# Optimization experiments

Hardware: AMD Instinct MI355X
Metric: run time of the kernel (lower is better)

Reference implementation:

```python
import jax, jax.numpy as jnp
import numpy as np

D, LEN_IN, LEN_OUT = 2, 1, 10
H1, H2 = 32, 32
B, T = 4096, 512
F_IN = D * LEN_IN          # 2
F_OUT = D * LEN_OUT        # 20


def setup_inputs() -> dict:
    key = jax.random.key(0)
    ks = jax.random.split(key, 12)
    s = 1.0 / np.sqrt(H1)  # PyTorch default init scale for LSTMCell/Linear
    u = lambda k, shape: jax.random.uniform(k, shape, jnp.float32, -s, s)
    return {
        "x": jax.random.normal(ks[0], (B, T, F_IN), jnp.float32),
        # LSTMCell 1 (input 2 -> hidden 32); gate order i,f,g,o stacked on dim 0
        "W_ih1": u(ks[1], (4 * H1, F_IN)),
        "W_hh1": u(ks[2], (4 * H1, H1)),
        "b_ih1": u(ks[3], (4 * H1,)),
        "b_hh1": u(ks[4], (4 * H1,)),
        # LSTMCell 2 (32 -> 32)
        "W_ih2": u(ks[5], (4 * H2, H1)),
        "W_hh2": u(ks[6], (4 * H2, H2)),
        "b_ih2": u(ks[7], (4 * H2,)),
        "b_hh2": u(ks[8], (4 * H2,)),
        # Final linear 32 -> 20
        "W_out": u(ks[9], (F_OUT, H2)),
        "b_out": u(ks[10], (F_OUT,)),
    }


def _lstm_cell(x, h, c, W_ih, W_hh, b):
    # gates: [B, 4H]; PyTorch gate order i, f, g, o
    gates = x @ W_ih.T + h @ W_hh.T + b
    i, f, g, o = jnp.split(gates, 4, axis=-1)
    i, f, o = jax.nn.sigmoid(i), jax.nn.sigmoid(f), jax.nn.sigmoid(o)
    g = jnp.tanh(g)
    c_new = f * c + i * g
    h_new = o * jnp.tanh(c_new)
    return h_new, c_new


def reference(x, W_ih1, W_hh1, b_ih1, b_hh1, W_ih2, W_hh2, b_ih2, b_hh2, W_out, b_out):
    b1 = b_ih1 + b_hh1
    b2 = b_ih2 + b_hh2
    Bsz = x.shape[0]
    h1 = jnp.zeros((Bsz, H1), x.dtype)
    c1 = jnp.zeros((Bsz, H1), x.dtype)
    h2 = jnp.zeros((Bsz, H2), x.dtype)
    c2 = jnp.zeros((Bsz, H2), x.dtype)

    def step(carry, x_t):
        h1, c1, h2, c2 = carry
        h1, c1 = _lstm_cell(x_t, h1, c1, W_ih1, W_hh1, b1)
        h2, c2 = _lstm_cell(h1, h2, c2, W_ih2, W_hh2, b2)
        out_t = h2 @ W_out.T + b_out  # [B, 20]
        return (h1, c1, h2, c2), out_t

    xs = jnp.swapaxes(x, 0, 1)  # [T, B, F_IN]
    _, outs = jax.lax.scan(step, (h1, c1, h2, c2), xs)  # outs: [T, B, 20]
    outs = jnp.swapaxes(outs, 0, 1)  # [B, T, 20]
    return outs.reshape(Bsz, x.shape[1], D, LEN_OUT)
```

## Files before the change

### kernel.cpp

```cpp
#include <hip/hip_runtime.h>
#include <hip/hip_fp16.h>

#define TLEN 512
#define HDIM 32
#define FOUT 20
#define HST  36

typedef __attribute__((ext_vector_type(8))) short bf16x8;
typedef __attribute__((ext_vector_type(4))) float f32x4;
typedef __attribute__((ext_vector_type(4))) short s16x4;

__device__ __forceinline__ float sigm(float v) {
  float e = __builtin_amdgcn_exp2f(-1.4426950408889634f * v);
  return __builtin_amdgcn_rcpf(1.0f + e);
}
__device__ __forceinline__ float tanh_f(float v) {
  float e = __builtin_amdgcn_exp2f(2.8853900817779268f * v);
  return 1.0f - 2.0f * __builtin_amdgcn_rcpf(1.0f + e);
}
__device__ __forceinline__ void hilo(float v, short& h, short& l) {
  unsigned u = __builtin_bit_cast(unsigned, v);
  unsigned r = u + 0x7fffu + ((u >> 16) & 1u);
  h = (short)(r >> 16);
  float hf = __builtin_bit_cast(float, r & 0xffff0000u);
  float res = v - hf;
  unsigned u2 = __builtin_bit_cast(unsigned, res);
  unsigned r2 = u2 + 0x7fffu + ((u2 >> 16) & 1u);
  l = (short)(r2 >> 16);
}

__device__ __forceinline__ void barrier_lgkm() {
  asm volatile("s_waitcnt lgkmcnt(0)\n\ts_barrier" ::: "memory");
}

__device__ __forceinline__ bf16x8 read_h(const short* buf, int off) {
  s16x4 a = *(const s16x4*)(buf + off);
  s16x4 b = *(const s16x4*)(buf + off + 4);
  bf16x8 r;
  r[0]=a[0]; r[1]=a[1]; r[2]=a[2]; r[3]=a[3];
  r[4]=b[0]; r[5]=b[1]; r[6]=b[2]; r[7]=b[3];
  return r;
}

__device__ __forceinline__ float lstm_update(const f32x4& g, float& c) {
  float iv = sigm(g[0]), fv = sigm(g[1]), gv = tanh_f(g[2]), ov = sigm(g[3]);
  c = fv * c + iv * gv;
  return ov * tanh_f(c);
}

__global__ __launch_bounds__(1024, 1) void lstm_seq_kernel(
    const float* __restrict__ xg,
    const float* __restrict__ Wih1, const float* __restrict__ Whh1,
    const float* __restrict__ bih1, const float* __restrict__ bhh1,
    const float* __restrict__ Wih2, const float* __restrict__ Whh2,
    const float* __restrict__ bih2, const float* __restrict__ bhh2,
    const float* __restrict__ Wout, const float* __restrict__ bout,
    float* __restrict__ out)
{
  __shared__ __half xl[16 * 1028];
  __shared__ short h1hiB[2][16 * HST], h1loB[2][16 * HST];
  __shared__ short h2hiB[2][16 * HST], h2loB[2][16 * HST];

  const int tid  = threadIdx.x;
  const int w    = tid >> 6;
  const int lane = tid & 63;
  const int n    = lane & 15;
  const int q    = lane >> 4;
  const int q4   = q * 4;
  const int q8   = q * 8;
  const int b0   = blockIdx.x * 16;
  const bool isL1 = (w < 8);
  const int wr   = w & 7;
  const int p    = w & 1;
  const int pr   = w >> 1;

  for (int idx = tid; idx < 16 * 1024; idx += 1024) {
    int row = idx >> 10, col = idx & 1023;
    xl[row * 1028 + col] = __float2half(xg[((size_t)(b0 + row) << 10) + col]);
  }

  const int og = (n & 3) * HDIM + 4 * wr + (n >> 2);
  bf16x8 WAh, WAl, WBh, WBl;
  float bc[4], wx0[4], wx1[4], boc[4];
  bf16x8 WoH = {0,0,0,0,0,0,0,0}, WoL = {0,0,0,0,0,0,0,0};
  if (isL1) {
    #pragma unroll
    for (int j = 0; j < 8; j++) {
      short hh, ll;
      hilo(Whh1[og * HDIM + q8 + j], hh, ll); WAh[j] = hh; WAl[j] = ll;
    }
    #pragma unroll
    for (int r = 0; r < 4; r++) {
      int gr = r * HDIM + 4 * wr + q;
      bc[r]  = bih1[gr] + bhh1[gr];
      wx0[r] = Wih1[gr * 2 + 0];
      wx1[r] = Wih1[gr * 2 + 1];
      int orow = 16 * p + q4 + r;
      boc[r] = (orow < FOUT) ? bout[orow] : 0.0f;
    }
    int orow = 16 * p + n;
    if (orow < FOUT) {
      #pragma unroll
      for (int j = 0; j < 8; j++) {
        short hh, ll;
        hilo(Wout[orow * HDIM + q8 + j], hh, ll); WoH[j] = hh; WoL[j] = ll;
      }
    }
  } else {
    #pragma unroll
    for (int j = 0; j < 8; j++) {
      short hh, ll;
      hilo(Wih2[og * HDIM + q8 + j], hh, ll); WAh[j] = hh; WAl[j] = ll;
      hilo(Whh2[og * HDIM + q8 + j], hh, ll); WBh[j] = hh; WBl[j] = ll;
    }
    #pragma unroll
    for (int r = 0; r < 4; r++) {
      int gr = r * HDIM + 4 * wr + q;
      bc[r] = bih2[gr] + bhh2[gr];
    }
  }

  const int hoff = n * HST + 4 * wr + q;
  const int aoff = n * HST + q8;
  float c = 0.0f;

  bf16x8 h1h = {0,0,0,0,0,0,0,0}, h1l = {0,0,0,0,0,0,0,0};
  bf16x8 h2h = {0,0,0,0,0,0,0,0}, h2l = {0,0,0,0,0,0,0,0};

  __syncthreads();

  if (isL1) {
    __half2 hv = *(const __half2*)&xl[n * 1028];
    float xv0 = __half2float(hv.x), xv1 = __half2float(hv.y);
    f32x4 g1;
    #pragma unroll
    for (int r = 0; r < 4; r++) g1[r] = fmaf(xv1, wx1[r], fmaf(xv0, wx0[r], bc[r]));
    float h1n = lstm_update(g1, c);
    short hh, ll; hilo(h1n, hh, ll);
    h1hiB[0][hoff] = hh; h1loB[0][hoff] = ll;
  }
  barrier_lgkm();
  h1h = read_h(h1hiB[0], aoff);
  h1l = read_h(h1loB[0], aoff);

  for (int t = 1; t < TLEN; ++t) {
    const int par = t & 1;
    if (isL1) {
      __half2 hv = *(const __half2*)&xl[n * 1028 + 2 * t];
      float xv0 = __half2float(hv.x), xv1 = __half2float(hv.y);

      f32x4 g1;
      #pragma unroll
      for (int r = 0; r < 4; r++) g1[r] = fmaf(xv1, wx1[r], fmaf(xv0, wx0[r], bc[r]));
      g1 = __builtin_amdgcn_mfma_f32_16x16x32_bf16(WAh, h1h, g1, 0, 0, 0);
      g1 = __builtin_amdgcn_mfma_f32_16x16x32_bf16(WAl, h1h, g1, 0, 0, 0);
      g1 = __builtin_amdgcn_mfma_f32_16x16x32_bf16(WAh, h1l, g1, 0, 0, 0);

      float h1n = lstm_update(g1, c);
      short hh, ll; hilo(h1n, hh, ll);
      h1hiB[par][hoff] = hh; h1loB[par][hoff] = ll;

      const int s = t - 2;
      if (s >= 0 && pr == (s & 3)) {
        f32x4 ao;
        #pragma unroll
        for (int r = 0; r < 4; r++) ao[r] = boc[r];
        ao = __builtin_amdgcn_mfma_f32_16x16x32_bf16(WoH, h2h, ao, 0, 0, 0);
        ao = __builtin_amdgcn_mfma_f32_16x16x32_bf16(WoL, h2h, ao, 0, 0, 0);
        ao = __builtin_amdgcn_mfma_f32_16x16x32_bf16(WoH, h2l, ao, 0, 0, 0);
        if (p == 0 || q == 0) {
          float4 st = { ao[0], ao[1], ao[2], ao[3] };
          *(float4*)&out[((size_t)(b0 + n) * TLEN + s) * FOUT + 16 * p + q4] = st;
        }
      }
    } else {
      f32x4 ga, gb;
      #pragma unroll
      for (int r = 0; r < 4; r++) { ga[r] = bc[r]; gb[r] = 0.0f; }
      ga = __builtin_amdgcn_mfma_f32_16x16x32_bf16(WAh, h1h, ga, 0, 0, 0);
      gb = __builtin_amdgcn_mfma_f32_16x16x32_bf16(WBh, h2h, gb, 0, 0, 0);
      ga = __builtin_amdgcn_mfma_f32_16x16x32_bf16(WAl, h1h, ga, 0, 0, 0);
      gb = __builtin_amdgcn_mfma_f32_16x16x32_bf16(WBl, h2h, gb, 0, 0, 0);
      ga = __builtin_amdgcn_mfma_f32_16x16x32_bf16(WAh, h1l, ga, 0, 0, 0);
      gb = __builtin_amdgcn_mfma_f32_16x16x32_bf16(WBh, h2l, gb, 0, 0, 0);

      f32x4 g2;
      #pragma unroll
      for (int r = 0; r < 4; r++) g2[r] = ga[r] + gb[r];
      float h2n = lstm_update(g2, c);
      short hh, ll; hilo(h2n, hh, ll);
      h2hiB[par][hoff] = hh; h2loB[par][hoff] = ll;
    }

    barrier_lgkm();

    h1h = read_h(h1hiB[par], aoff);
    h1l = read_h(h1loB[par], aoff);
    if (!isL1 || pr == ((t - 1) & 3)) {
      h2h = read_h(h2hiB[par], aoff);
      h2l = read_h(h2loB[par], aoff);
    }
  }

  if (!isL1) {
    f32x4 ga, gb;
    #pragma unroll
    for (int r = 0; r < 4; r++) { ga[r] = bc[r]; gb[r] = 0.0f; }
    ga = __builtin_amdgcn_mfma_f32_16x16x32_bf16(WAh, h1h, ga, 0, 0, 0);
    gb = __builtin_amdgcn_mfma_f32_16x16x32_bf16(WBh, h2h, gb, 0, 0, 0);
    ga = __builtin_amdgcn_mfma_f32_16x16x32_bf16(WAl, h1h, ga, 0, 0, 0);
    gb = __builtin_amdgcn_mfma_f32_16x16x32_bf16(WBl, h2h, gb, 0, 0, 0);
    ga = __builtin_amdgcn_mfma_f32_16x16x32_bf16(WAh, h1l, ga, 0, 0, 0);
    gb = __builtin_amdgcn_mfma_f32_16x16x32_bf16(WBh, h2l, gb, 0, 0, 0);
    f32x4 g2;
    #pragma unroll
    for (int r = 0; r < 4; r++) g2[r] = ga[r] + gb[r];
    float h2n = lstm_update(g2, c);
    short hh, ll; hilo(h2n, hh, ll);
    h2hiB[0][hoff] = hh; h2loB[0][hoff] = ll;
  } else if (pr == 2) {
    const int s = TLEN - 2;
    f32x4 ao;
    #pragma unroll
    for (int r = 0; r < 4; r++) ao[r] = boc[r];
    ao = __builtin_amdgcn_mfma_f32_16x16x32_bf16(WoH, h2h, ao, 0, 0, 0);
    ao = __builtin_amdgcn_mfma_f32_16x16x32_bf16(WoL, h2h, ao, 0, 0, 0);
    ao = __builtin_amdgcn_mfma_f32_16x16x32_bf16(WoH, h2l, ao, 0, 0, 0);
    if (p == 0 || q == 0) {
      float4 st = { ao[0], ao[1], ao[2], ao[3] };
      *(float4*)&out[((size_t)(b0 + n) * TLEN + s) * FOUT + 16 * p + q4] = st;
    }
  }
  barrier_lgkm();

  if (isL1 && pr == 3) {
    h2h = read_h(h2hiB[0], aoff);
    h2l = read_h(h2loB[0], aoff);
    const int s = TLEN - 1;
    f32x4 ao;
    #pragma unroll
    for (int r = 0; r < 4; r++) ao[r] = boc[r];
    ao = __builtin_amdgcn_mfma_f32_16x16x32_bf16(WoH, h2h, ao, 0, 0, 0);
    ao = __builtin_amdgcn_mfma_f32_16x16x32_bf16(WoL, h2h, ao, 0, 0, 0);
    ao = __builtin_amdgcn_mfma_f32_16x16x32_bf16(WoH, h2l, ao, 0, 0, 0);
    if (p == 0 || q == 0) {
      float4 st = { ao[0], ao[1], ao[2], ao[3] };
      *(float4*)&out[((size_t)(b0 + n) * TLEN + s) * FOUT + 16 * p + q4] = st;
    }
  }
}

extern "C" void kernel_launch(void* const* d_in, const int* in_sizes, int n_in,
                              void* d_out, int out_size, void* d_ws, size_t ws_size,
                              hipStream_t stream) {
  const float* xg   = (const float*)d_in[0];
  const float* Wih1 = (const float*)d_in[1];
  const float* Whh1 = (const float*)d_in[2];
  const float* bih1 = (const float*)d_in[3];
  const float* bhh1 = (const float*)d_in[4];
  const float* Wih2 = (const float*)d_in[5];
  const float* Whh2 = (const float*)d_in[6];
  const float* bih2 = (const float*)d_in[7];
  const float* bhh2 = (const float*)d_in[8];
  const float* Wout = (const float*)d_in[9];
  const float* bout = (const float*)d_in[10];
  float* out = (float*)d_out;

  hipLaunchKernelGGL(lstm_seq_kernel, dim3(256), dim3(1024), 0, stream,
                     xg, Wih1, Whh1, bih1, bhh1, Wih2, Whh2, bih2, bhh2, Wout, bout, out);
}
```

Baseline: 494.3 us.

## Unroll LSTM time loop by four and move output projection after barrier

The timestep loop is unrolled by four through a STEP macro, so parity and rotating-row indices become compile-time constants, and the x inputs for four steps come from two vector LDS loads. The hidden-state row stride grows from 36 to 40 shorts so each read_h becomes a single aligned 8-element LDS load instead of two 4-element loads. The output-projection MFMAs and global stores now run after the barrier instead of before it, taking them off the critical path to the barrier. The risks are higher register pressure and code size from the unrolling, and possible LDS bank conflicts from the new stride.

Result: faster. 442.4 us (-10.5%).

```diff
diff --git a/kernel.cpp b/kernel.cpp
--- a/kernel.cpp
+++ b/kernel.cpp
@@ -4,7 +4,7 @@
 #define TLEN 512
 #define HDIM 32
 #define FOUT 20
-#define HST  36
+#define HST  40
 
 typedef __attribute__((ext_vector_type(8))) short bf16x8;
 typedef __attribute__((ext_vector_type(4))) float f32x4;
@@ -34,12 +34,7 @@
 }
 
 __device__ __forceinline__ bf16x8 read_h(const short* buf, int off) {
-  s16x4 a = *(const s16x4*)(buf + off);
-  s16x4 b = *(const s16x4*)(buf + off + 4);
-  bf16x8 r;
-  r[0]=a[0]; r[1]=a[1]; r[2]=a[2]; r[3]=a[3];
-  r[4]=b[0]; r[5]=b[1]; r[6]=b[2]; r[7]=b[3];
-  return r;
+  return *(const bf16x8*)(buf + off);
 }
 
 __device__ __forceinline__ float lstm_update(const f32x4& g, float& c) {
@@ -143,64 +138,82 @@
   h1h = read_h(h1hiB[0], aoff);
   h1l = read_h(h1loB[0], aoff);
 
-  for (int t = 1; t < TLEN; ++t) {
-    const int par = t & 1;
+#define STEP(T, PAR, DS3, HR3, XV0, XV1)                                          \
+  {                                                                               \
+    if (isL1) {                                                                   \
+      f32x4 g1;                                                                   \
+      _Pragma("unroll") for (int r = 0; r < 4; r++)                               \
+        g1[r] = fmaf((XV1), wx1[r], fmaf((XV0), wx0[r], bc[r]));                  \
+      g1 = __builtin_amdgcn_mfma_f32_16x16x32_bf16(WAh, h1h, g1, 0, 0, 0);        \
+      g1 = __builtin_amdgcn_mfma_f32_16x16x32_bf16(WAl, h1h, g1, 0, 0, 0);        \
+      g1 = __builtin_amdgcn_mfma_f32_16x16x32_bf16(WAh, h1l, g1, 0, 0, 0);        \
+      float h1n = lstm_update(g1, c);                                             \
+      short hh, ll; hilo(h1n, hh, ll);                                            \
+      h1hiB[PAR][hoff] = hh; h1loB[PAR][hoff] = ll;                               \
+    } else {                                                                      \
+      f32x4 ga, gb;                                                               \
+      _Pragma("unroll") for (int r = 0; r < 4; r++) { ga[r] = bc[r]; gb[r] = 0.0f; } \
+      ga = __builtin_amdgcn_mfma_f32_16x16x32_bf16(WAh, h1h, ga, 0, 0, 0);        \
+      gb = __builtin_amdgcn_mfma_f32_16x16x32_bf16(WBh, h2h, gb, 0, 0, 0);        \
+      ga = __builtin_amdgcn_mfma_f32_16x16x32_bf16(WAl, h1h, ga, 0, 0, 0);        \
+      gb = __builtin_amdgcn_mfma_f32_16x16x32_bf16(WBl, h2h, gb, 0, 0, 0);        \
+      ga = __builtin_amdgcn_mfma_f32_16x16x32_bf16(WAh, h1l, ga, 0, 0, 0);        \
+      gb = __builtin_amdgcn_mfma_f32_16x16x32_bf16(WBh, h2l, gb, 0, 0, 0);        \
+      f32x4 g2;                                                                   \
+      _Pragma("unroll") for (int r = 0; r < 4; r++) g2[r] = ga[r] + gb[r];        \
+      float h2n = lstm_update(g2, c);                                             \
+      short hh, ll; hilo(h2n, hh, ll);                                            \
+      h2hiB[PAR][hoff] = hh; h2loB[PAR][hoff] = ll;                               \
+    }                                                                             \
+    barrier_lgkm();                                   \
+    h1h = read_h(h1hiB[PAR], aoff);                                               \
+    h1l = read_h(h1loB[PAR], aoff);                                               \
+                    \
+    if ((DS3) >= 0 && isL1 && pr == (DS3)) {                                      \
+      f32x4 ao;                                                                   \
+      _Pragma("unroll") for (int r = 0; r < 4; r++) ao[r] = boc[r];               \
+      ao = __builtin_amdgcn_mfma_f32_16x16x32_bf16(WoH, h2h, ao, 0, 0, 0);        \
+      ao = __builtin_amdgcn_mfma_f32_16x16x32_bf16(WoL, h2h, ao, 0, 0, 0);        \
+      ao = __builtin_amdgcn_mfma_f32_16x16x32_bf16(WoH, h2l, ao, 0, 0, 0);        \
+      if (p == 0 || q == 0) {                                                     \
+        float4 st = { ao[0], ao[1], ao[2], ao[3] };                               \
+        *(float4*)&out[((size_t)(b0 + n) * TLEN + ((T) - 2)) * FOUT + 16 * p + q4] = st; \
+      }                                                                           \
+    }                                                                             \
+    if (!isL1 || pr == (HR3)) {                                                   \
+      h2h = read_h(h2hiB[PAR], aoff);                                             \
+      h2l = read_h(h2loB[PAR], aoff);                                             \
+    }                                                                             \
+  }
+
+  {
+    float a0 = 0.f, a1 = 0.f;
+    if (isL1) { __half2 hv = *(const __half2*)&xl[n * 1028 + 2]; a0 = __half2float(hv.x); a1 = __half2float(hv.y); }
+    STEP(1, 1, -1, 0, a0, a1);
+    if (isL1) { __half2 hv = *(const __half2*)&xl[n * 1028 + 4]; a0 = __half2float(hv.x); a1 = __half2float(hv.y); }
+    STEP(2, 0, 0, 1, a0, a1);
+    if (isL1) { __half2 hv = *(const __half2*)&xl[n * 1028 + 6]; a0 = __half2float(hv.x); a1 = __half2float(hv.y); }
+    STEP(3, 1, 1, 2, a0, a1);
+  }
+
+  for (int t = 4; t < TLEN; t += 4) {
+    float xv[8] = {0.f, 0.f, 0.f, 0.f, 0.f, 0.f, 0.f, 0.f};
     if (isL1) {
-      __half2 hv = *(const __half2*)&xl[n * 1028 + 2 * t];
-      float xv0 = __half2float(hv.x), xv1 = __half2float(hv.y);
-
-      f32x4 g1;
+      const short* xp = (const short*)xl + n * 1028 + 2 * t;
+      s16x4 xa = *(const s16x4*)xp;
+      s16x4 xb = *(const s16x4*)(xp + 4);
       #pragma unroll
-      for (int r = 0; r < 4; r++) g1[r] = fmaf(xv1, wx1[r], fmaf(xv0, wx0[r], bc[r]));
-      g1 = __builtin_amdgcn_mfma_f32_16x16x32_bf16(WAh, h1h, g1, 0, 0, 0);
-      g1 = __builtin_amdgcn_mfma_f32_16x16x32_bf16(WAl, h1h, g1, 0, 0, 0);
-      g1 = __builtin_amdgcn_mfma_f32_16x16x32_bf16(WAh, h1l, g1, 0, 0, 0);
-
-      float h1n = lstm_update(g1, c);
-      short hh, ll; hilo(h1n, hh, ll);
-      h1hiB[par][hoff] = hh; h1loB[par][hoff] = ll;
-
-      const int s = t - 2;
-      if (s >= 0 && pr == (s & 3)) {
-        f32x4 ao;
-        #pragma unroll
-        for (int r = 0; r < 4; r++) ao[r] = boc[r];
-        ao = __builtin_amdgcn_mfma_f32_16x16x32_bf16(WoH, h2h, ao, 0, 0, 0);
-        ao = __builtin_amdgcn_mfma_f32_16x16x32_bf16(WoL, h2h, ao, 0, 0, 0);
-        ao = __builtin_amdgcn_mfma_f32_16x16x32_bf16(WoH, h2l, ao, 0, 0, 0);
-        if (p == 0 || q == 0) {
-          float4 st = { ao[0], ao[1], ao[2], ao[3] };
-          *(float4*)&out[((size_t)(b0 + n) * TLEN + s) * FOUT + 16 * p + q4] = st;
-        }
+      for (int j = 0; j < 4; j++) {
+        xv[j]     = __half2float(__builtin_bit_cast(__half, (short)xa[j]));
+        xv[4 + j] = __half2float(__builtin_bit_cast(__half, (short)xb[j]));
       }
-    } else {
-      f32x4 ga, gb;
-      #pragma unroll
-      for (int r = 0; r < 4; r++) { ga[r] = bc[r]; gb[r] = 0.0f; }
-      ga = __builtin_amdgcn_mfma_f32_16x16x32_bf16(WAh, h1h, ga, 0, 0, 0);
-      gb = __builtin_amdgcn_mfma_f32_16x16x32_bf16(WBh, h2h, gb, 0, 0, 0);
-      ga = __builtin_amdgcn_mfma_f32_16x16x32_bf16(WAl, h1h, ga, 0, 0, 0);
-      gb = __builtin_amdgcn_mfma_f32_16x16x32_bf16(WBl, h2h, gb, 0, 0, 0);
-      ga = __builtin_amdgcn_mfma_f32_16x16x32_bf16(WAh, h1l, ga, 0, 0, 0);
-      gb = __builtin_amdgcn_mfma_f32_16x16x32_bf16(WBh, h2l, gb, 0, 0, 0);
-
-      f32x4 g2;
-      #pragma unroll
-      for (int r = 0; r < 4; r++) g2[r] = ga[r] + gb[r];
-      float h2n = lstm_update(g2, c);
-      short hh, ll; hilo(h2n, hh, ll);
-      h2hiB[par][hoff] = hh; h2loB[par][hoff] = ll;
-    }
-
-    barrier_lgkm();
-
-    h1h = read_h(h1hiB[par], aoff);
-    h1l = read_h(h1loB[par], aoff);
-    if (!isL1 || pr == ((t - 1) & 3)) {
-      h2h = read_h(h2hiB[par], aoff);
-      h2l = read_h(h2loB[par], aoff);
-    }
-  }
+    }
+    STEP(t + 0, 0, 2, 3, xv[0], xv[1]);
+    STEP(t + 1, 1, 3, 0, xv[2], xv[3]);
+    STEP(t + 2, 0, 0, 1, xv[4], xv[5]);
+    STEP(t + 3, 1, 1, 2, xv[6], xv[7]);
+  }
+#undef STEP
 
   if (!isL1) {
     f32x4 ga, gb;
```
